# Optimization experiments

Measured on AMD Instinct MI355X. Metric: run time of the kernel, lower is better.

The kernel has to match this reference:

```python
import jax, jax.numpy as jnp
import numpy as np

N_NODES = 100_000
N_EDGES = 3_200_000
N_FEAT = 128
N_HID = 8
N_CLASSES = 10


def setup_inputs() -> dict:
    key = jax.random.key(0)
    ks = jax.random.split(key, 16)
    g = lambda k, shape, fan_in: jax.random.normal(k, shape, jnp.float32) / np.sqrt(fan_in)
    inp = {}
    inp['x'] = jax.random.normal(ks[0], (N_NODES, N_FEAT), jnp.float32)
    inp['edge_index'] = jax.random.randint(ks[1], (2, N_EDGES), 0, N_NODES, jnp.int32)
    # lin: Linear(F, 8)
    inp['lin_w'] = g(ks[2], (N_FEAT, N_HID), N_FEAT)
    inp['lin_b'] = jnp.zeros((N_HID,), jnp.float32)
    # conv1: GATConv(8, 8, heads=2)
    inp['w1'] = g(ks[3], (N_HID, 2 * N_HID), N_HID)
    inp['a1_src'] = g(ks[4], (2, N_HID), N_HID)
    inp['a1_dst'] = g(ks[5], (2, N_HID), N_HID)
    inp['b1'] = jnp.zeros((2 * N_HID,), jnp.float32)
    # conv2: GATConv(16, 8, heads=2)
    inp['w2'] = g(ks[6], (2 * N_HID, 2 * N_HID), 2 * N_HID)
    inp['a2_src'] = g(ks[7], (2, N_HID), N_HID)
    inp['a2_dst'] = g(ks[8], (2, N_HID), N_HID)
    inp['b2'] = jnp.zeros((2 * N_HID,), jnp.float32)
    # conv3: GATConv(16, num_classes, heads=1, concat=False)
    inp['w3'] = g(ks[9], (2 * N_HID, N_CLASSES), 2 * N_HID)
    inp['a3_src'] = g(ks[10], (1, N_CLASSES), N_CLASSES)
    inp['a3_dst'] = g(ks[11], (1, N_CLASSES), N_CLASSES)
    inp['b3'] = jnp.zeros((N_CLASSES,), jnp.float32)
    return inp


def _gat_conv(x, W, a_src, a_dst, b, src, dst, heads, out_c, concat):
    """PyG GATConv with pre-appended self-loops in (src, dst)."""
    N = x.shape[0]
    xl = (x @ W).reshape(N, heads, out_c)                 # [N,H,C]
    alpha_src = (xl * a_src[None]).sum(-1)                # [N,H]
    alpha_dst = (xl * a_dst[None]).sum(-1)                # [N,H]
    e = jax.nn.leaky_relu(alpha_src[src] + alpha_dst[dst], 0.2)  # [E,H]
    # segment softmax over destination nodes
    m = jax.ops.segment_max(e, dst, num_segments=N)
    e = jnp.exp(e - m[dst])
    s = jax.ops.segment_sum(e, dst, num_segments=N)
    alpha = e / s[dst]                                    # [E,H]
    msg = xl[src] * alpha[:, :, None]                     # [E,H,C]
    out = jax.ops.segment_sum(msg, dst, num_segments=N)   # [N,H,C]
    out = out.reshape(N, heads * out_c) if concat else out.mean(axis=1)
    return out + b


def reference(x, edge_index, lin_w, lin_b, w1, a1_src, a1_dst, b1,
              w2, a2_src, a2_dst, b2, w3, a3_src, a3_dst, b3):
    N = x.shape[0]
    loops = jnp.arange(N, dtype=edge_index.dtype)
    src = jnp.concatenate([edge_index[0], loops])
    dst = jnp.concatenate([edge_index[1], loops])
    lrelu = lambda v: jax.nn.leaky_relu(v, 0.01)
    h = lrelu(x @ lin_w + lin_b)
    h = lrelu(_gat_conv(h, w1, a1_src, a1_dst, b1, src, dst, 2, N_HID, True))
    h = lrelu(_gat_conv(h, w2, a2_src, a2_dst, b2, src, dst, 2, N_HID, True))
    h = _gat_conv(h, w3, a3_src, a3_dst, b3, src, dst, 1, N_CLASSES, False)
    return jax.nn.log_softmax(h, axis=-1)
```

## Files before the change

### kernel.cpp

```cpp
#include <hip/hip_runtime.h>
#include <hip/hip_fp16.h>
#include <math.h>

#define N_NODES 100000
#define N_EDGES 3200000
#define ET (N_EDGES + N_NODES)
#define SLOT 80
#define KMAX 5
#define SHIFT 8
#define BNODES 256
#define NBUCK 391
#define BCAP 9088
#define P1_T 1024
#define E_PER 16
#define P1_WG ((N_EDGES + P1_T * E_PER - 1) / (P1_T * E_PER))
#define SCAN_T 1024
#define SCAN_CHUNK 98

__device__ __forceinline__ float lrelu(float v, float s) { return v > 0.f ? v : v * s; }

template <int CTRL>
__device__ __forceinline__ float dppmov(float v) {
    return __int_as_float(__builtin_amdgcn_update_dpp(0, __float_as_int(v), CTRL, 0xF, 0xF, true));
}

__device__ __forceinline__ void reduce16(float& v, float& ssum, float pa0, float pa1,
                                         float pa2, float pa3, int lane) {
    int b0 = lane & 1, b1 = (lane >> 1) & 1;
    float k0 = b0 ? pa2 : pa0, g0 = b0 ? pa0 : pa2;
    float k1 = b0 ? pa3 : pa1, g1 = b0 ? pa1 : pa3;
    float q0 = k0 + dppmov<0xB1>(g0);
    float q1 = k1 + dppmov<0xB1>(g1);
    float kk = b1 ? q1 : q0, gg = b1 ? q0 : q1;
    v = kk + dppmov<0x4E>(gg);
    v += __shfl_xor(v, 4, 64);
    v += __shfl_xor(v, 8, 64);
    ssum += dppmov<0xB1>(ssum);
    ssum += dppmov<0x4E>(ssum);
    ssum += __shfl_xor(ssum, 4, 64);
    ssum += __shfl_xor(ssum, 8, 64);
}

__global__ __launch_bounds__(256) void lin_kernel(const float* __restrict__ x,
                                                  const float* __restrict__ w,
                                                  const float* __restrict__ b,
                                                  float* __restrict__ h0) {
    int lane = threadIdx.x & 63;
    int wid = blockIdx.x * 4 + (threadIdx.x >> 6);
    float4 wa0 = *(const float4*)&w[lane * 8];
    float4 wa1 = *(const float4*)&w[lane * 8 + 4];
    float4 wb0 = *(const float4*)&w[(lane + 64) * 8];
    float4 wb1 = *(const float4*)&w[(lane + 64) * 8 + 4];
    float wk0[8] = {wa0.x, wa0.y, wa0.z, wa0.w, wa1.x, wa1.y, wa1.z, wa1.w};
    float wk1[8] = {wb0.x, wb0.y, wb0.z, wb0.w, wb1.x, wb1.y, wb1.z, wb1.w};
    int l = lane & 7;
    int kmap = 4 * (l & 1) + 2 * ((l >> 1) & 1) + ((l >> 2) & 1);
    float bk = b[kmap];
#pragma unroll
    for (int j = 0; j < 4; j++) {
        int n = wid * 4 + j;
        if (n >= N_NODES) break;
        float x0 = x[n * 128 + lane];
        float x1 = x[n * 128 + 64 + lane];
        float acc[8];
#pragma unroll
        for (int k = 0; k < 8; k++) acc[k] = x0 * wk0[k] + x1 * wk1[k];
#pragma unroll
        for (int k = 0; k < 4; k++) {
            float keep = (lane & 1) ? acc[k + 4] : acc[k];
            float give = (lane & 1) ? acc[k] : acc[k + 4];
            acc[k] = keep + __shfl_xor(give, 1, 64);
        }
#pragma unroll
        for (int k = 0; k < 2; k++) {
            float keep = (lane & 2) ? acc[k + 2] : acc[k];
            float give = (lane & 2) ? acc[k] : acc[k + 2];
            acc[k] = keep + __shfl_xor(give, 2, 64);
        }
        {
            float keep = (lane & 4) ? acc[1] : acc[0];
            float give = (lane & 4) ? acc[0] : acc[1];
            acc[0] = keep + __shfl_xor(give, 4, 64);
        }
        acc[0] += __shfl_xor(acc[0], 8, 64);
        acc[0] += __shfl_xor(acc[0], 16, 64);
        acc[0] += __shfl_xor(acc[0], 32, 64);
        if (lane < 8) h0[n * 8 + kmap] = lrelu(acc[0] + bk, 0.01f);
    }
}

__global__ void __launch_bounds__(P1_T) part_kernel(const int* __restrict__ ei,
                                                    int* __restrict__ bcur,
                                                    unsigned* __restrict__ pairs) {
    __shared__ int hist[NBUCK];
    __shared__ int gbase[NBUCK];
    int t = threadIdx.x;
    for (int i = t; i < NBUCK; i += P1_T) hist[i] = 0;
    __syncthreads();
    int base = blockIdx.x * (P1_T * E_PER);
    int s[E_PER], d[E_PER], r[E_PER];
#pragma unroll
    for (int k = 0; k < E_PER; k++) {
        int e = base + k * P1_T + t;
        if (e < N_EDGES) {
            s[k] = ei[e];
            d[k] = ei[N_EDGES + e];
            r[k] = atomicAdd(&hist[d[k] >> SHIFT], 1);
        }
    }
    __syncthreads();
    for (int i = t; i < NBUCK; i += P1_T)
        gbase[i] = (hist[i] > 0) ? atomicAdd(&bcur[i], hist[i]) : 0;
    __syncthreads();
#pragma unroll
    for (int k = 0; k < E_PER; k++) {
        int e = base + k * P1_T + t;
        if (e < N_EDGES) {
            int b = d[k] >> SHIFT;
            int pos = gbase[b] + r[k];
            if (pos < BCAP)
                pairs[(size_t)b * BCAP + pos] =
                    ((unsigned)(d[k] & (BNODES - 1)) << 17) | (unsigned)s[k];
        }
    }
}

__global__ void build_kernel(const int* __restrict__ bcur, const unsigned* __restrict__ pairs,
                             int* __restrict__ csr, int* __restrict__ deg) {
    __shared__ int offs[BNODES];
    int b = blockIdx.x;
    int t = threadIdx.x;
    int node0 = b << SHIFT;
    int n = node0 + t;
    if (n < N_NODES) {
        csr[n * SLOT] = n;
        offs[t] = 1;
    } else offs[t] = 0;
    __syncthreads();
    int cnt = min(bcur[b], BCAP);
    for (int i = t; i < cnt; i += BNODES) {
        unsigned v = pairs[(size_t)b * BCAP + i];
        int ln = v >> 17;
        int s = v & 0x1FFFF;
        int pos = atomicAdd(&offs[ln], 1);
        if (pos < SLOT) csr[(node0 + ln) * SLOT + pos] = s;
    }
    __syncthreads();
    if (n < N_NODES) deg[n] = offs[t];
}

__global__ void count_kernel(const int* __restrict__ ei, int* __restrict__ deg) {
    int e = blockIdx.x * blockDim.x + threadIdx.x;
    if (e >= ET) return;
    int d = (e < N_EDGES) ? ei[N_EDGES + e] : (e - N_EDGES);
    atomicAdd(&deg[d], 1);
}

__global__ void scan_kernel(const int* __restrict__ deg, int* __restrict__ rowptr,
                            int* __restrict__ cursor) {
    __shared__ int sums[SCAN_T];
    int t = threadIdx.x;
    int start = t * SCAN_CHUNK;
    int end = min(start + SCAN_CHUNK, N_NODES);
    int s = 0;
    for (int i = start; i < end; i++) s += deg[i];
    sums[t] = s;
    __syncthreads();
    for (int off = 1; off < SCAN_T; off <<= 1) {
        int v = sums[t];
        int add = (t >= off) ? sums[t - off] : 0;
        __syncthreads();
        sums[t] = v + add;
        __syncthreads();
    }
    int base = (t > 0) ? sums[t - 1] : 0;
    for (int i = start; i < end; i++) {
        rowptr[i] = base;
        cursor[i] = base;
        base += deg[i];
    }
    if (t == SCAN_T - 1) rowptr[N_NODES] = base;
}

__global__ void scatter_kernel(const int* __restrict__ ei, int* __restrict__ cursor,
                               int* __restrict__ csr) {
    int e = blockIdx.x * blockDim.x + threadIdx.x;
    if (e >= ET) return;
    int s, d;
    if (e < N_EDGES) { s = ei[e]; d = ei[N_EDGES + e]; } else { s = d = e - N_EDGES; }
    int pos = atomicAdd(&cursor[d], 1);
    csr[pos] = s;
}

template <int CIN, int H, int C, int XLS>
__global__ void prep_kernel(const float* __restrict__ hin, const float* __restrict__ W,
                            const float* __restrict__ a_src, const float* __restrict__ a_dst,
                            __half* __restrict__ xl, float* __restrict__ asrc,
                            float* __restrict__ adst) {
    __shared__ float Ws[CIN * H * C];
    __shared__ float As[H * C];
    __shared__ float Ad[H * C];
    for (int i = threadIdx.x; i < CIN * H * C; i += blockDim.x) Ws[i] = W[i];
    for (int i = threadIdx.x; i < H * C; i += blockDim.x) { As[i] = a_src[i]; Ad[i] = a_dst[i]; }
    __syncthreads();
    int n = blockIdx.x * blockDim.x + threadIdx.x;
    if (n >= N_NODES) return;
    float hreg[CIN];
#pragma unroll
    for (int i = 0; i < CIN; i += 4) {
        float4 v = *(const float4*)&hin[n * CIN + i];
        hreg[i] = v.x; hreg[i + 1] = v.y; hreg[i + 2] = v.z; hreg[i + 3] = v.w;
    }
#pragma unroll
    for (int h = 0; h < H; h++) {
        float as = 0.f, ad = 0.f;
#pragma unroll
        for (int c = 0; c < C; c++) {
            float v = 0.f;
#pragma unroll
            for (int i = 0; i < CIN; i++) v += hreg[i] * Ws[i * H * C + h * C + c];
            xl[n * XLS + h * C + c] = __float2half_rn(v);
            as += v * As[h * C + c];
            ad += v * Ad[h * C + c];
        }
        asrc[n * H + h] = as;
        adst[n * H + h] = ad;
    }
#pragma unroll
    for (int c = H * C; c < XLS; c++) xl[n * XLS + c] = __float2half_rn(0.f);
}

__global__ __launch_bounds__(256) void gat64_h2(const int* __restrict__ cnt_,
                                                const int* __restrict__ csr,
                                                const float* __restrict__ a_src,
                                                const float* __restrict__ adst,
                                                const __half* __restrict__ xl,
                                                const float* __restrict__ b,
                                                float* __restrict__ hout) {
    int wg = blockIdx.x * 4 + (threadIdx.x >> 6);
    int lane = threadIdx.x & 63;
    int eg = lane & 15;
    int cp = lane >> 4;
    int h = cp >> 1;
    int n0 = wg * 2, n1 = n0 + 1;
    float4 asv = *(const float4*)&a_src[4 * cp];
    int cnt0 = min(cnt_[n0], SLOT);
    int cnt1 = min(cnt_[n1], SLOT);
    float ad0 = adst[n0 * 2 + h];
    float ad1 = adst[n1 * 2 + h];
    int idx0[KMAX], idx1[KMAX];
#pragma unroll
    for (int k = 0; k < KMAX; k++) {
        int i = eg + (k << 4);
        idx0[k] = (i < cnt0) ? csr[n0 * SLOT + i] : -1;
        idx1[k] = (i < cnt1) ? csr[n1 * SLOT + i] : -1;
    }
    float s0 = 0.f, a00 = 0.f, a01 = 0.f, a02 = 0.f, a03 = 0.f;
    float s1 = 0.f, a10 = 0.f, a11 = 0.f, a12 = 0.f, a13 = 0.f;
#pragma unroll
    for (int k = 0; k < KMAX; k++) {
        int s = idx0[k];
        if (s >= 0) {
            float2 raw = *(const float2*)&xl[s * 16 + 4 * cp];
            float2 f01 = __half22float2(*(__half2*)&raw.x);
            float2 f23 = __half22float2(*(__half2*)&raw.y);
            float part = f01.x * asv.x + f01.y * asv.y + f23.x * asv.z + f23.y * asv.w;
            float as = part + __shfl_xor(part, 16, 64);
            float e = as + ad0;
            float w = __expf(fmaxf(e, 0.2f * e));
            s0 += w;
            a00 += w * f01.x; a01 += w * f01.y; a02 += w * f23.x; a03 += w * f23.y;
        }
        int t = idx1[k];
        if (t >= 0) {
            float2 raw = *(const float2*)&xl[t * 16 + 4 * cp];
            float2 f01 = __half22float2(*(__half2*)&raw.x);
            float2 f23 = __half22float2(*(__half2*)&raw.y);
            float part = f01.x * asv.x + f01.y * asv.y + f23.x * asv.z + f23.y * asv.w;
            float as = part + __shfl_xor(part, 16, 64);
            float e = as + ad1;
            float w = __expf(fmaxf(e, 0.2f * e));
            s1 += w;
            a10 += w * f01.x; a11 += w * f01.y; a12 += w * f23.x; a13 += w * f23.y;
        }
    }
    float v0, v1;
    reduce16(v0, s0, a00, a01, a02, a03, lane);
    reduce16(v1, s1, a10, a11, a12, a13, lane);
    if ((lane & 12) == 0) {
        int ch = 4 * cp + 2 * (lane & 1) + ((lane >> 1) & 1);
        float bc = b[ch];
        hout[n0 * 16 + ch] = lrelu(v0 / s0 + bc, 0.01f);
        hout[n1 * 16 + ch] = lrelu(v1 / s1 + bc, 0.01f);
    }
}

__global__ __launch_bounds__(256) void gat64_ls(const int* __restrict__ cnt_,
                                                const int* __restrict__ csr,
                                                const float* __restrict__ a_src,
                                                const float* __restrict__ adst,
                                                const __half* __restrict__ xl,
                                                const float* __restrict__ b,
                                                float* __restrict__ out) {
    int wg = blockIdx.x * 4 + (threadIdx.x >> 6);
    int lane = threadIdx.x & 63;
    int eg = lane & 15;
    int cp = lane >> 4;
    int n0 = wg * 2, n1 = n0 + 1;
    float4 asv;
    {
        int c0 = 4 * cp;
        asv.x = (c0 + 0 < 10) ? a_src[c0 + 0] : 0.f;
        asv.y = (c0 + 1 < 10) ? a_src[c0 + 1] : 0.f;
        asv.z = (c0 + 2 < 10) ? a_src[c0 + 2] : 0.f;
        asv.w = (c0 + 3 < 10) ? a_src[c0 + 3] : 0.f;
    }
    int cnt0 = min(cnt_[n0], SLOT);
    int cnt1 = min(cnt_[n1], SLOT);
    float ad0 = adst[n0];
    float ad1 = adst[n1];
    int idx0[KMAX], idx1[KMAX];
#pragma unroll
    for (int k = 0; k < KMAX; k++) {
        int i = eg + (k << 4);
        idx0[k] = (i < cnt0) ? csr[n0 * SLOT + i] : -1;
        idx1[k] = (i < cnt1) ? csr[n1 * SLOT + i] : -1;
    }
    float s0 = 0.f, a00 = 0.f, a01 = 0.f, a02 = 0.f, a03 = 0.f;
    float s1 = 0.f, a10 = 0.f, a11 = 0.f, a12 = 0.f, a13 = 0.f;
#pragma unroll
    for (int k = 0; k < KMAX; k++) {
        int s = idx0[k];
        if (s >= 0) {
            float2 raw = *(const float2*)&xl[s * 16 + 4 * cp];
            float2 f01 = __half22float2(*(__half2*)&raw.x);
            float2 f23 = __half22float2(*(__half2*)&raw.y);
            float part = f01.x * asv.x + f01.y * asv.y + f23.x * asv.z + f23.y * asv.w;
            part += __shfl_xor(part, 16, 64);
            part += __shfl_xor(part, 32, 64);
            float e = part + ad0;
            float w = __expf(fmaxf(e, 0.2f * e));
            s0 += w;
            a00 += w * f01.x; a01 += w * f01.y; a02 += w * f23.x; a03 += w * f23.y;
        }
        int t = idx1[k];
        if (t >= 0) {
            float2 raw = *(const float2*)&xl[t * 16 + 4 * cp];
            float2 f01 = __half22float2(*(__half2*)&raw.x);
            float2 f23 = __half22float2(*(__half2*)&raw.y);
            float part = f01.x * asv.x + f01.y * asv.y + f23.x * asv.z + f23.y * asv.w;
            part += __shfl_xor(part, 16, 64);
            part += __shfl_xor(part, 32, 64);
            float e = part + ad1;
            float w = __expf(fmaxf(e, 0.2f * e));
            s1 += w;
            a10 += w * f01.x; a11 += w * f01.y; a12 += w * f23.x; a13 += w * f23.y;
        }
    }
    float v0, v1;
    reduce16(v0, s0, a00, a01, a02, a03, lane);
    reduce16(v1, s1, a10, a11, a12, a13, lane);
    int ch = 4 * cp + 2 * (lane & 1) + ((lane >> 1) & 1);
    float bc = (ch < 10) ? b[ch] : 0.f;
    float u0 = (ch < 10) ? v0 / s0 + bc : -INFINITY;
    float u1 = (ch < 10) ? v1 / s1 + bc : -INFINITY;
    float m0 = u0, m1 = u1;
    m0 = fmaxf(m0, dppmov<0xB1>(m0)); m1 = fmaxf(m1, dppmov<0xB1>(m1));
    m0 = fmaxf(m0, dppmov<0x4E>(m0)); m1 = fmaxf(m1, dppmov<0x4E>(m1));
    m0 = fmaxf(m0, __shfl_xor(m0, 16, 64)); m1 = fmaxf(m1, __shfl_xor(m1, 16, 64));
    m0 = fmaxf(m0, __shfl_xor(m0, 32, 64)); m1 = fmaxf(m1, __shfl_xor(m1, 32, 64));
    float e0 = (ch < 10) ? __expf(u0 - m0) : 0.f;
    float e1 = (ch < 10) ? __expf(u1 - m1) : 0.f;
    e0 += dppmov<0xB1>(e0); e1 += dppmov<0xB1>(e1);
    e0 += dppmov<0x4E>(e0); e1 += dppmov<0x4E>(e1);
    e0 += __shfl_xor(e0, 16, 64); e1 += __shfl_xor(e1, 16, 64);
    e0 += __shfl_xor(e0, 32, 64); e1 += __shfl_xor(e1, 32, 64);
    float lse0 = m0 + __logf(e0);
    float lse1 = m1 + __logf(e1);
    if ((lane & 12) == 0 && ch < 10) {
        out[n0 * 10 + ch] = u0 - lse0;
        out[n1 * 10 + ch] = u1 - lse1;
    }
}

__global__ void gat16_h2(const int* __restrict__ rowptr, const int* __restrict__ csr,
                         const float* __restrict__ asrc, const float* __restrict__ adst,
                         const __half* __restrict__ xl, const float* __restrict__ b,
                         float* __restrict__ hout) {
    int tid = blockIdx.x * blockDim.x + threadIdx.x;
    int wave = tid >> 6;
    int lane = threadIdx.x & 63;
    int g = lane >> 4;
    int c = lane & 15;
    int h = c >> 3;
    int n = wave * 4 + g;
    if (n >= N_NODES) return;
    int beg = rowptr[n], cnt = rowptr[n + 1] - beg;
    float adn = adst[n * 2 + h];
    float ssum = 0.f, pa = 0.f;
#pragma unroll 4
    for (int i = 0; i < cnt; i++) {
        int s = csr[beg + i];
        float e = asrc[s * 2 + h] + adn;
        float w = __expf(fmaxf(e, 0.2f * e));
        ssum += w;
        pa += w * __half2float(xl[s * 16 + c]);
    }
    hout[n * 16 + c] = lrelu(pa / ssum + b[c], 0.01f);
}

__global__ void gat16_ls(const int* __restrict__ rowptr, const int* __restrict__ csr,
                         const float* __restrict__ asrc, const float* __restrict__ adst,
                         const __half* __restrict__ xl, const float* __restrict__ b,
                         float* __restrict__ out) {
    int tid = blockIdx.x * blockDim.x + threadIdx.x;
    int wave = tid >> 6;
    int lane = threadIdx.x & 63;
    int g = lane >> 4;
    int c = lane & 15;
    int n = wave * 4 + g;
    if (n >= N_NODES) return;
    int beg = rowptr[n], cnt = rowptr[n + 1] - beg;
    float adn = adst[n];
    float ssum = 0.f, pa = 0.f;
#pragma unroll 4
    for (int i = 0; i < cnt; i++) {
        int s = csr[beg + i];
        float e = asrc[s] + adn;
        float w = __expf(fmaxf(e, 0.2f * e));
        ssum += w;
        pa += w * __half2float(xl[s * 16 + c]);
    }
    float v = pa / ssum + ((c < 10) ? b[c] : 0.f);
    float vm = (c < 10) ? v : -INFINITY;
#pragma unroll
    for (int off = 8; off >= 1; off >>= 1) vm = fmaxf(vm, __shfl_xor(vm, off, 16));
    float ex = (c < 10) ? __expf(v - vm) : 0.f;
    float sum = ex;
#pragma unroll
    for (int off = 8; off >= 1; off >>= 1) sum += __shfl_xor(sum, off, 16);
    float lse = vm + __logf(sum);
    if (c < 10) out[n * 10 + c] = v - lse;
}

extern "C" void kernel_launch(void* const* d_in, const int* in_sizes, int n_in,
                              void* d_out, int out_size, void* d_ws, size_t ws_size,
                              hipStream_t stream) {
    const float* x     = (const float*)d_in[0];
    const int*   ei    = (const int*)d_in[1];
    const float* lin_w = (const float*)d_in[2];
    const float* lin_b = (const float*)d_in[3];
    const float* w1    = (const float*)d_in[4];
    const float* a1s   = (const float*)d_in[5];
    const float* a1d   = (const float*)d_in[6];
    const float* b1    = (const float*)d_in[7];
    const float* w2    = (const float*)d_in[8];
    const float* a2s   = (const float*)d_in[9];
    const float* a2d   = (const float*)d_in[10];
    const float* b2    = (const float*)d_in[11];
    const float* w3    = (const float*)d_in[12];
    const float* a3s   = (const float*)d_in[13];
    const float* a3d   = (const float*)d_in[14];
    const float* b3    = (const float*)d_in[15];

    float* ws = (float*)d_ws;
    float* slotH  = ws;
    __half* slotX = (__half*)(ws + 1600000);
    float* as_    = ws + 3200000;
    float* ad_    = ws + 3400000;
    unsigned* pairs = (unsigned*)ws;
    int* csrP = (int*)(ws + 3600000);
    int* degP = (int*)(ws + 3600000 + N_NODES * SLOT);
    int* bcur = degP + N_NODES;
    size_t need_new = (size_t)(3600000 + N_NODES * SLOT + N_NODES + 512) * 4;

    int use_bucket = (ws_size >= need_new) ? 1 : 0;

    int* degC    = (int*)(ws + 3600000);
    int* rowptrC = degC + N_NODES;
    int* cursorC = rowptrC + N_NODES + 1;
    int* csrC    = cursorC + N_NODES;

    dim3 B(256);
    int nb_n  = (N_NODES + 255) / 256;
    int nb_et = (ET + 255) / 256;
    int nb_g  = (N_NODES + 15) / 16;
    int nb_w2 = N_NODES / 8;

    if (use_bucket) {
        hipMemsetAsync(bcur, 0, 512 * sizeof(int), stream);
        part_kernel<<<P1_WG, P1_T, 0, stream>>>(ei, bcur, pairs);
        build_kernel<<<NBUCK, BNODES, 0, stream>>>(bcur, pairs, csrP, degP);
    } else {
        hipMemsetAsync(degC, 0, N_NODES * sizeof(int), stream);
        count_kernel<<<nb_et, B, 0, stream>>>(ei, degC);
        scan_kernel<<<1, SCAN_T, 0, stream>>>(degC, rowptrC, cursorC);
        scatter_kernel<<<nb_et, B, 0, stream>>>(ei, cursorC, csrC);
    }

    lin_kernel<<<dim3((N_NODES + 15) / 16), B, 0, stream>>>(x, lin_w, lin_b, slotH);

    prep_kernel<8, 2, 8, 16><<<nb_n, B, 0, stream>>>(slotH, w1, a1s, a1d, slotX, as_, ad_);
    if (use_bucket) gat64_h2<<<nb_w2, B, 0, stream>>>(degP, csrP, a1s, ad_, slotX, b1, slotH);
    else            gat16_h2<<<nb_g, B, 0, stream>>>(rowptrC, csrC, as_, ad_, slotX, b1, slotH);

    prep_kernel<16, 2, 8, 16><<<nb_n, B, 0, stream>>>(slotH, w2, a2s, a2d, slotX, as_, ad_);
    if (use_bucket) gat64_h2<<<nb_w2, B, 0, stream>>>(degP, csrP, a2s, ad_, slotX, b2, slotH);
    else            gat16_h2<<<nb_g, B, 0, stream>>>(rowptrC, csrC, as_, ad_, slotX, b2, slotH);

    prep_kernel<16, 1, 10, 16><<<nb_n, B, 0, stream>>>(slotH, w3, a3s, a3d, slotX, as_, ad_);
    if (use_bucket) gat64_ls<<<nb_w2, B, 0, stream>>>(degP, csrP, a3s, ad_, slotX, b3, (float*)d_out);
    else            gat16_ls<<<nb_g, B, 0, stream>>>(rowptrC, csrC, as_, ad_, slotX, b3, (float*)d_out);
}
```

Baseline: 302.8 us.

## Fuse linear layer into first GAT prep, batch gathers, use exp2 with prescaled logits

Removes the separate lin_kernel and computes the 128->8 linear layer plus leaky-relu inside a new prep kernel, which then feeds the first GAT projection, saving one launch and an intermediate write and read. The gather kernels now issue all index loads and feature loads up front, bounded by a wave-uniform chunk count, and mask out-of-range edges with zero weight instead of branching per edge. Exponentials switch to the native exp2 with attention vectors pre-scaled by log2(e). The fused prep makes each thread read a full 512-byte row of x, which is less coalesced than the old per-wave layout, and holding the gathered values up front raises register use.

```diff
diff --git a/kernel.cpp b/kernel.cpp
--- a/kernel.cpp
+++ b/kernel.cpp
@@ -16,8 +16,10 @@
 #define P1_WG ((N_EDGES + P1_T * E_PER - 1) / (P1_T * E_PER))
 #define SCAN_T 1024
 #define SCAN_CHUNK 98
+#define LOG2E 1.44269504088896f
 
 __device__ __forceinline__ float lrelu(float v, float s) { return v > 0.f ? v : v * s; }
+__device__ __forceinline__ float fexp2(float x) { return __builtin_amdgcn_exp2f(x); }
 
 template <int CTRL>
 __device__ __forceinline__ float dppmov(float v) {
@@ -41,54 +43,6 @@
     ssum += __shfl_xor(ssum, 8, 64);
 }
 
-__global__ __launch_bounds__(256) void lin_kernel(const float* __restrict__ x,
-                                                  const float* __restrict__ w,
-                                                  const float* __restrict__ b,
-                                                  float* __restrict__ h0) {
-    int lane = threadIdx.x & 63;
-    int wid = blockIdx.x * 4 + (threadIdx.x >> 6);
-    float4 wa0 = *(const float4*)&w[lane * 8];
-    float4 wa1 = *(const float4*)&w[lane * 8 + 4];
-    float4 wb0 = *(const float4*)&w[(lane + 64) * 8];
-    float4 wb1 = *(const float4*)&w[(lane + 64) * 8 + 4];
-    float wk0[8] = {wa0.x, wa0.y, wa0.z, wa0.w, wa1.x, wa1.y, wa1.z, wa1.w};
-    float wk1[8] = {wb0.x, wb0.y, wb0.z, wb0.w, wb1.x, wb1.y, wb1.z, wb1.w};
-    int l = lane & 7;
-    int kmap = 4 * (l & 1) + 2 * ((l >> 1) & 1) + ((l >> 2) & 1);
-    float bk = b[kmap];
-#pragma unroll
-    for (int j = 0; j < 4; j++) {
-        int n = wid * 4 + j;
-        if (n >= N_NODES) break;
-        float x0 = x[n * 128 + lane];
-        float x1 = x[n * 128 + 64 + lane];
-        float acc[8];
-#pragma unroll
-        for (int k = 0; k < 8; k++) acc[k] = x0 * wk0[k] + x1 * wk1[k];
-#pragma unroll
-        for (int k = 0; k < 4; k++) {
-            float keep = (lane & 1) ? acc[k + 4] : acc[k];
-            float give = (lane & 1) ? acc[k] : acc[k + 4];
-            acc[k] = keep + __shfl_xor(give, 1, 64);
-        }
-#pragma unroll
-        for (int k = 0; k < 2; k++) {
-            float keep = (lane & 2) ? acc[k + 2] : acc[k];
-            float give = (lane & 2) ? acc[k] : acc[k + 2];
-            acc[k] = keep + __shfl_xor(give, 2, 64);
-        }
-        {
-            float keep = (lane & 4) ? acc[1] : acc[0];
-            float give = (lane & 4) ? acc[0] : acc[1];
-            acc[0] = keep + __shfl_xor(give, 4, 64);
-        }
-        acc[0] += __shfl_xor(acc[0], 8, 64);
-        acc[0] += __shfl_xor(acc[0], 16, 64);
-        acc[0] += __shfl_xor(acc[0], 32, 64);
-        if (lane < 8) h0[n * 8 + kmap] = lrelu(acc[0] + bk, 0.01f);
-    }
-}
-
 __global__ void __launch_bounds__(P1_T) part_kernel(const int* __restrict__ ei,
                                                     int* __restrict__ bcur,
                                                     unsigned* __restrict__ pairs) {
@@ -201,7 +155,10 @@
     __shared__ float As[H * C];
     __shared__ float Ad[H * C];
     for (int i = threadIdx.x; i < CIN * H * C; i += blockDim.x) Ws[i] = W[i];
-    for (int i = threadIdx.x; i < H * C; i += blockDim.x) { As[i] = a_src[i]; Ad[i] = a_dst[i]; }
+    for (int i = threadIdx.x; i < H * C; i += blockDim.x) {
+        As[i] = a_src[i] * LOG2E;
+        Ad[i] = a_dst[i] * LOG2E;
+    }
     __syncthreads();
     int n = blockIdx.x * blockDim.x + threadIdx.x;
     if (n >= N_NODES) return;
@@ -219,6 +176,63 @@
             float v = 0.f;
 #pragma unroll
             for (int i = 0; i < CIN; i++) v += hreg[i] * Ws[i * H * C + h * C + c];
+            xl[n * XLS + h * C + c] = __float2half_rn(v);
+            as += v * As[h * C + c];
+            ad += v * Ad[h * C + c];
+        }
+        asrc[n * H + h] = as;
+        adst[n * H + h] = ad;
+    }
+#pragma unroll
+    for (int c = H * C; c < XLS; c++) xl[n * XLS + c] = __float2half_rn(0.f);
+}
+
+template <int H, int C, int XLS>
+__global__ __launch_bounds__(256) void prep_lin_kernel(
+        const float* __restrict__ x, const float* __restrict__ lw, const float* __restrict__ lb,
+        const float* __restrict__ W, const float* __restrict__ a_src,
+        const float* __restrict__ a_dst, __half* __restrict__ xl,
+        float* __restrict__ asrc, float* __restrict__ adst) {
+    __shared__ float LW[128 * 8];
+    __shared__ float Ws[8 * H * C];
+    __shared__ float As[H * C];
+    __shared__ float Ad[H * C];
+    __shared__ float Lb[8];
+    for (int i = threadIdx.x; i < 128 * 8; i += 256) LW[i] = lw[i];
+    for (int i = threadIdx.x; i < 8 * H * C; i += 256) Ws[i] = W[i];
+    for (int i = threadIdx.x; i < H * C; i += 256) {
+        As[i] = a_src[i] * LOG2E;
+        Ad[i] = a_dst[i] * LOG2E;
+    }
+    if (threadIdx.x < 8) Lb[threadIdx.x] = lb[threadIdx.x];
+    __syncthreads();
+    int n = blockIdx.x * blockDim.x + threadIdx.x;
+    if (n >= N_NODES) return;
+    float hreg[8];
+#pragma unroll
+    for (int c = 0; c < 8; c++) hreg[c] = 0.f;
+#pragma unroll 8
+    for (int i = 0; i < 128; i += 4) {
+        float4 v = *(const float4*)&x[n * 128 + i];
+#pragma unroll
+        for (int c = 0; c < 8; c++) hreg[c] += v.x * LW[(i + 0) * 8 + c];
+#pragma unroll
+        for (int c = 0; c < 8; c++) hreg[c] += v.y * LW[(i + 1) * 8 + c];
+#pragma unroll
+        for (int c = 0; c < 8; c++) hreg[c] += v.z * LW[(i + 2) * 8 + c];
+#pragma unroll
+        for (int c = 0; c < 8; c++) hreg[c] += v.w * LW[(i + 3) * 8 + c];
+    }
+#pragma unroll
+    for (int c = 0; c < 8; c++) hreg[c] = lrelu(hreg[c] + Lb[c], 0.01f);
+#pragma unroll
+    for (int h = 0; h < H; h++) {
+        float as = 0.f, ad = 0.f;
+#pragma unroll
+        for (int c = 0; c < C; c++) {
+            float v = 0.f;
+#pragma unroll
+            for (int i = 0; i < 8; i++) v += hreg[i] * Ws[i * H * C + h * C + c];
             xl[n * XLS + h * C + c] = __float2half_rn(v);
             as += v * As[h * C + c];
             ad += v * Ad[h * C + c];
@@ -244,42 +258,54 @@
     int h = cp >> 1;
     int n0 = wg * 2, n1 = n0 + 1;
     float4 asv = *(const float4*)&a_src[4 * cp];
+    asv.x *= LOG2E; asv.y *= LOG2E; asv.z *= LOG2E; asv.w *= LOG2E;
     int cnt0 = min(cnt_[n0], SLOT);
     int cnt1 = min(cnt_[n1], SLOT);
+    int ka0 = __builtin_amdgcn_readfirstlane((cnt0 + 15) >> 4);
+    int ka1 = __builtin_amdgcn_readfirstlane((cnt1 + 15) >> 4);
     float ad0 = adst[n0 * 2 + h];
     float ad1 = adst[n1 * 2 + h];
     int idx0[KMAX], idx1[KMAX];
 #pragma unroll
     for (int k = 0; k < KMAX; k++) {
-        int i = eg + (k << 4);
-        idx0[k] = (i < cnt0) ? csr[n0 * SLOT + i] : -1;
-        idx1[k] = (i < cnt1) ? csr[n1 * SLOT + i] : -1;
+        if (k < ka0) idx0[k] = csr[n0 * SLOT + eg + (k << 4)];
+        if (k < ka1) idx1[k] = csr[n1 * SLOT + eg + (k << 4)];
+    }
+    float2 raw0[KMAX], raw1[KMAX];
+#pragma unroll
+    for (int k = 0; k < KMAX; k++) {
+        if (k < ka0) {
+            int s = (eg + (k << 4) < cnt0) ? idx0[k] : 0;
+            raw0[k] = *(const float2*)&xl[s * 16 + 4 * cp];
+        }
+        if (k < ka1) {
+            int t = (eg + (k << 4) < cnt1) ? idx1[k] : 0;
+            raw1[k] = *(const float2*)&xl[t * 16 + 4 * cp];
+        }
     }
     float s0 = 0.f, a00 = 0.f, a01 = 0.f, a02 = 0.f, a03 = 0.f;
     float s1 = 0.f, a10 = 0.f, a11 = 0.f, a12 = 0.f, a13 = 0.f;
 #pragma unroll
     for (int k = 0; k < KMAX; k++) {
-        int s = idx0[k];
-        if (s >= 0) {
-            float2 raw = *(const float2*)&xl[s * 16 + 4 * cp];
-            float2 f01 = __half22float2(*(__half2*)&raw.x);
-            float2 f23 = __half22float2(*(__half2*)&raw.y);
+        if (k < ka0) {
+            float2 f01 = __half22float2(*(__half2*)&raw0[k].x);
+            float2 f23 = __half22float2(*(__half2*)&raw0[k].y);
             float part = f01.x * asv.x + f01.y * asv.y + f23.x * asv.z + f23.y * asv.w;
             float as = part + __shfl_xor(part, 16, 64);
             float e = as + ad0;
-            float w = __expf(fmaxf(e, 0.2f * e));
+            float w = fexp2(fmaxf(e, 0.2f * e));
+            w = (eg + (k << 4) < cnt0) ? w : 0.f;
             s0 += w;
             a00 += w * f01.x; a01 += w * f01.y; a02 += w * f23.x; a03 += w * f23.y;
         }
-        int t = idx1[k];
-        if (t >= 0) {
-            float2 raw = *(const float2*)&xl[t * 16 + 4 * cp];
-            float2 f01 = __half22float2(*(__half2*)&raw.x);
-            float2 f23 = __half22float2(*(__half2*)&raw.y);
+        if (k < ka1) {
+            float2 f01 = __half22float2(*(__half2*)&raw1[k].x);
+            float2 f23 = __half22float2(*(__half2*)&raw1[k].y);
             float part = f01.x * asv.x + f01.y * asv.y + f23.x * asv.z + f23.y * asv.w;
             float as = part + __shfl_xor(part, 16, 64);
             float e = as + ad1;
-            float w = __expf(fmaxf(e, 0.2f * e));
+            float w = fexp2(fmaxf(e, 0.2f * e));
+            w = (eg + (k << 4) < cnt1) ? w : 0.f;
             s1 += w;
             a10 += w * f01.x; a11 += w * f01.y; a12 += w * f23.x; a13 += w * f23.y;
         }
@@ -310,49 +336,60 @@
     float4 asv;
     {
         int c0 = 4 * cp;
-        asv.x = (c0 + 0 < 10) ? a_src[c0 + 0] : 0.f;
-        asv.y = (c0 + 1 < 10) ? a_src[c0 + 1] : 0.f;
-        asv.z = (c0 + 2 < 10) ? a_src[c0 + 2] : 0.f;
-        asv.w = (c0 + 3 < 10) ? a_src[c0 + 3] : 0.f;
+        asv.x = (c0 + 0 < 10) ? a_src[c0 + 0] * LOG2E : 0.f;
+        asv.y = (c0 + 1 < 10) ? a_src[c0 + 1] * LOG2E : 0.f;
+        asv.z = (c0 + 2 < 10) ? a_src[c0 + 2] * LOG2E : 0.f;
+        asv.w = (c0 + 3 < 10) ? a_src[c0 + 3] * LOG2E : 0.f;
     }
     int cnt0 = min(cnt_[n0], SLOT);
     int cnt1 = min(cnt_[n1], SLOT);
+    int ka0 = __builtin_amdgcn_readfirstlane((cnt0 + 15) >> 4);
+    int ka1 = __builtin_amdgcn_readfirstlane((cnt1 + 15) >> 4);
     float ad0 = adst[n0];
     float ad1 = adst[n1];
     int idx0[KMAX], idx1[KMAX];
 #pragma unroll
     for (int k = 0; k < KMAX; k++) {
-        int i = eg + (k << 4);
-        idx0[k] = (i < cnt0) ? csr[n0 * SLOT + i] : -1;
-        idx1[k] = (i < cnt1) ? csr[n1 * SLOT + i] : -1;
+        if (k < ka0) idx0[k] = csr[n0 * SLOT + eg + (k << 4)];
+        if (k < ka1) idx1[k] = csr[n1 * SLOT + eg + (k << 4)];
+    }
+    float2 raw0[KMAX], raw1[KMAX];
+#pragma unroll
+    for (int k = 0; k < KMAX; k++) {
+        if (k < ka0) {
+            int s = (eg + (k << 4) < cnt0) ? idx0[k] : 0;
+            raw0[k] = *(const float2*)&xl[s * 16 + 4 * cp];
+        }
+        if (k < ka1) {
+            int t = (eg + (k << 4) < cnt1) ? idx1[k] : 0;
+            raw1[k] = *(const float2*)&xl[t * 16 + 4 * cp];
+        }
     }
     float s0 = 0.f, a00 = 0.f, a01 = 0.f, a02 = 0.f, a03 = 0.f;
     float s1 = 0.f, a10 = 0.f, a11 = 0.f, a12 = 0.f, a13 = 0.f;
 #pragma unroll
     for (int k = 0; k < KMAX; k++) {
-        int s = idx0[k];
-        if (s >= 0) {
-            float2 raw = *(const float2*)&xl[s * 16 + 4 * cp];
-            float2 f01 = __half22float2(*(__half2*)&raw.x);
-            float2 f23 = __half22float2(*(__half2*)&raw.y);
+        if (k < ka0) {
+            float2 f01 = __half22float2(*(__half2*)&raw0[k].x);
+            float2 f23 = __half22float2(*(__half2*)&raw0[k].y);
             float part = f01.x * asv.x + f01.y * asv.y + f23.x * asv.z + f23.y * asv.w;
             part += __shfl_xor(part, 16, 64);
             part += __shfl_xor(part, 32, 64);
             float e = part + ad0;
-            float w = __expf(fmaxf(e, 0.2f * e));
+            float w = fexp2(fmaxf(e, 0.2f * e));
+            w = (eg + (k << 4) < cnt0) ? w : 0.f;
             s0 += w;
             a00 += w * f01.x; a01 += w * f01.y; a02 += w * f23.x; a03 += w * f23.y;
         }
-        int t = idx1[k];
-        if (t >= 0) {
-            float2 raw = *(const float2*)&xl[t * 16 + 4 * cp];
-            float2 f01 = __half22float2(*(__half2*)&raw.x);
-            float2 f23 = __half22float2(*(__half2*)&raw.y);
+        if (k < ka1) {
+            float2 f01 = __half22float2(*(__half2*)&raw1[k].x);
+            float2 f23 = __half22float2(*(__half2*)&raw1[k].y);
             float part = f01.x * asv.x + f01.y * asv.y + f23.x * asv.z + f23.y * asv.w;
             part += __shfl_xor(part, 16, 64);
             part += __shfl_xor(part, 32, 64);
             float e = part + ad1;
-            float w = __expf(fmaxf(e, 0.2f * e));
+            float w = fexp2(fmaxf(e, 0.2f * e));
+            w = (eg + (k << 4) < cnt1) ? w : 0.f;
             s1 += w;
             a10 += w * f01.x; a11 += w * f01.y; a12 += w * f23.x; a13 += w * f23.y;
         }
@@ -402,7 +439,7 @@
     for (int i = 0; i < cnt; i++) {
         int s = csr[beg + i];
         float e = asrc[s * 2 + h] + adn;
-        float w = __expf(fmaxf(e, 0.2f * e));
+        float w = fexp2(fmaxf(e, 0.2f * e));
         ssum += w;
         pa += w * __half2float(xl[s * 16 + c]);
     }
@@ -427,7 +464,7 @@
     for (int i = 0; i < cnt; i++) {
         int s = csr[beg + i];
         float e = asrc[s] + adn;
-        float w = __expf(fmaxf(e, 0.2f * e));
+        float w = fexp2(fmaxf(e, 0.2f * e));
         ssum += w;
         pa += w * __half2float(xl[s * 16 + c]);
     }
@@ -498,9 +535,8 @@
         scatter_kernel<<<nb_et, B, 0, stream>>>(ei, cursorC, csrC);
     }
 
-    lin_kernel<<<dim3((N_NODES + 15) / 16), B, 0, stream>>>(x, lin_w, lin_b, slotH);
-
-    prep_kernel<8, 2, 8, 16><<<nb_n, B, 0, stream>>>(slotH, w1, a1s, a1d, slotX, as_, ad_);
+    prep_lin_kernel<2, 8, 16><<<nb_n, B, 0, stream>>>(x, lin_w, lin_b, w1, a1s, a1d,
+                                                      slotX, as_, ad_);
     if (use_bucket) gat64_h2<<<nb_w2, B, 0, stream>>>(degP, csrP, a1s, ad_, slotX, b1, slotH);
     else            gat16_h2<<<nb_g, B, 0, stream>>>(rowptrC, csrC, as_, ad_, slotX, b1, slotH);
 
```

New measurement: 296.6 us. 1.02x faster.
